# Kernel tuning notes

Hardware: AMD Instinct MI355X
Metric: run time of the kernel (lower is better)

## Reference

```python
import jax, jax.numpy as jnp
import numpy as np

B, T, D = 32, 200, 256
H, DH = 4, 32
INNER = H * DH  # 128
L, FF, NI = 8, 1024, 100000
NB = 64  # gap/recency buckets


def _ln(x, g, b, eps=1e-5):
    m = x.mean(-1, keepdims=True)
    v = jnp.mean((x - m) ** 2, -1, keepdims=True)
    return (x - m) / jnp.sqrt(v + eps) * g + b


def _gelu(x):
    return jax.nn.gelu(x, approximate=False)


def _dwconv_causal(x, w, b):
    # x: [B,T,C], w: [C,k] depthwise kernel, causal left-pad (k-1)
    k = w.shape[1]
    xp = jnp.pad(x, ((0, 0), (k - 1, 0), (0, 0))).transpose(0, 2, 1)  # [B,C,T+k-1]
    out = jax.lax.conv_general_dilated(
        xp, w[:, None, :], (1,), 'VALID',
        dimension_numbers=('NCH', 'OIH', 'NCH'), feature_group_count=w.shape[0])
    return out.transpose(0, 2, 1) + b


def _causal_linear_attention(q, k, v, m4):
    q = (jax.nn.elu(q) + 1.0) * m4
    k = (jax.nn.elu(k) + 1.0) * m4
    v = v * m4
    kv = jnp.einsum('bthd,bthe->bthde', k, v)          # [B,T,H,DH,DH]
    kv_prefix = jnp.cumsum(kv, axis=1)
    k_prefix = jnp.cumsum(k, axis=1)
    num = jnp.einsum('bthd,bthde->bthe', q, kv_prefix)
    den = jnp.sum(q * k_prefix, -1, keepdims=True)
    return num / (den + 1e-6) * m4


def _forward(item_emb, pos_emb, gap_emb, rec_emb, tf_w1, tf_b1, tf_w2, tf_b2,
             in_g, in_b, l_ln1g, l_ln1b, l_win, l_bin, l_wc, l_bc, l_tw, l_tb,
             l_pw, l_pb, l_wmix, l_bmix, l_ln2g, l_ln2b, l_wf1, l_bf1, l_wf2, l_bf2,
             fn_g, fn_b, pg_w, pg_b, uh_w1, uh_b1, uh_lng, uh_lnb, uh_w2, uh_b2,
             item_bias, ids, ts, lens):
    Bb, Tt = ids.shape
    pos = jnp.arange(Tt)
    mask = pos[None, :] >= (Tt - lens)[:, None]  # right-aligned valid mask [B,T]
    prev_ts = jnp.roll(ts, 1, axis=1)
    prev_mask = jnp.roll(mask, 1, axis=1).at[:, 0].set(False)
    zero = jnp.zeros_like(ts)
    gap_vals = jnp.where(mask & prev_mask, jnp.maximum(ts - prev_ts, 0), zero)
    latest = ts[:, -1:]
    rec_vals = jnp.where(mask, jnp.maximum(latest - ts, 0), zero)

    def buck(v, n):
        vf = jnp.maximum(v.astype(jnp.float32), 0.0)
        return jnp.clip(jnp.floor(jnp.log2(vf + 1.0)), 0, n - 1).astype(jnp.int32)

    gb = buck(gap_vals, NB)
    rb = buck(rec_vals, NB)
    rec_raw = jnp.maximum(latest - ts, 0).astype(jnp.float32)
    tf = jnp.stack([jnp.log1p(gb.astype(jnp.float32)), jnp.log1p(rec_raw)], -1)  # [B,T,2]
    dense_time = _gelu(tf @ tf_w1 + tf_b1) @ tf_w2 + tf_b2

    x = item_emb[ids] + pos_emb[None] + gap_emb[gb] + rec_emb[rb] + dense_time
    mf = mask[..., None].astype(x.dtype)
    m4 = mask[..., None, None].astype(x.dtype)
    x = _ln(x, in_g, in_b) * mf

    for i in range(L):
        res = x
        nrm = _ln(x, l_ln1g[i], l_ln1b[i])
        proj = nrm @ l_win[i] + l_bin[i]  # [B,T,D+3*INNER]
        gate = proj[..., :D]
        q = proj[..., D:D + INNER].reshape(Bb, Tt, H, DH)
        k = proj[..., D + INNER:D + 2 * INNER].reshape(Bb, Tt, H, DH)
        v = proj[..., D + 2 * INNER:].reshape(Bb, Tt, H, DH)
        content = _causal_linear_attention(q, k, v, m4).reshape(Bb, Tt, INNER) @ l_wc[i] + l_bc[i]
        temporal = _dwconv_causal(nrm, l_tw[i], l_tb[i])
        positional = _dwconv_causal(nrm, l_pw[i], l_pb[i])
        mixed = jnp.concatenate([content, temporal, positional], -1) @ l_wmix[i] + l_bmix[i]
        x = (res + jax.nn.sigmoid(gate) * mixed) * mf
        h = _ln(x, l_ln2g[i], l_ln2b[i])
        ffn = _gelu(h @ l_wf1[i] + l_bf1[i]) @ l_wf2[i] + l_bf2[i]
        x = (x + ffn) * mf

    x = _ln(x, fn_g, fn_b) * mf
    denom = jnp.maximum(lens, 1)[:, None].astype(x.dtype)
    mean_pooled = (x * mf).sum(1) / denom
    ps = (x @ pg_w + pg_b)[..., 0]
    ps = jnp.where(mask, ps, -1e9)
    pw = jax.nn.softmax(ps, axis=1)[..., None]
    attn_pooled = (pw * x).sum(1)
    last = x[:, -1, :]
    u = jnp.concatenate([last, mean_pooled, attn_pooled], -1)
    u = _gelu(u @ uh_w1 + uh_b1)
    u = _ln(u, uh_lng, uh_lnb)
    u = u @ uh_w2 + uh_b2
    u = u / jnp.maximum(jnp.linalg.norm(u, axis=-1, keepdims=True), 1e-12)
    ie = item_emb[1:]
    ie = ie / jnp.maximum(jnp.linalg.norm(ie, axis=-1, keepdims=True), 1e-12)
    return u @ ie.T + item_bias[1:]


def setup_inputs() -> dict:
    key = jax.random.key(0)
    it = iter(jax.random.split(key, 64))
    def nk():
        return next(it)
    def w(*s):
        return jax.random.normal(nk(), s, jnp.float32) * 0.02
    inp = dict(
        history_ids=jax.random.randint(nk(), (B, T), 0, NI),
        history_timestamps=jnp.sort(jax.random.randint(nk(), (B, T), 0, 1000000), axis=1),
        history_lengths=jax.random.randint(nk(), (B,), 1, T + 1),
        item_emb=w(NI + 1, D).at[0].set(0.0),
        pos_emb=w(T, D), gap_emb=w(NB, D), rec_emb=w(NB, D),
        tf_w1=w(2, D), tf_b1=jnp.zeros((D,)), tf_w2=w(D, D), tf_b2=jnp.zeros((D,)),
        in_g=jnp.ones((D,)), in_b=jnp.zeros((D,)),
        l_ln1g=jnp.ones((L, D)), l_ln1b=jnp.zeros((L, D)),
        l_win=w(L, D, D + 3 * INNER), l_bin=jnp.zeros((L, D + 3 * INNER)),
        l_wc=w(L, INNER, D), l_bc=jnp.zeros((L, D)),
        l_tw=w(L, D, 3), l_tb=jnp.zeros((L, D)),
        l_pw=w(L, D, 5), l_pb=jnp.zeros((L, D)),
        l_wmix=w(L, 3 * D, D), l_bmix=jnp.zeros((L, D)),
        l_ln2g=jnp.ones((L, D)), l_ln2b=jnp.zeros((L, D)),
        l_wf1=w(L, D, FF), l_bf1=jnp.zeros((L, FF)),
        l_wf2=w(L, FF, D), l_bf2=jnp.zeros((L, D)),
        fn_g=jnp.ones((D,)), fn_b=jnp.zeros((D,)),
        pg_w=w(D, 1), pg_b=jnp.zeros((1,)),
        uh_w1=w(3 * D, 1024), uh_b1=jnp.zeros((1024,)),
        uh_lng=jnp.ones((1024,)), uh_lnb=jnp.zeros((1024,)),
        uh_w2=w(1024, D), uh_b2=jnp.zeros((D,)),
        item_bias=jnp.zeros((NI + 1,)),
    )
    return inp


def reference(history_ids, history_timestamps, history_lengths, item_emb, pos_emb,
              gap_emb, rec_emb, tf_w1, tf_b1, tf_w2, tf_b2, in_g, in_b, l_ln1g,
              l_ln1b, l_win, l_bin, l_wc, l_bc, l_tw, l_tb, l_pw, l_pb, l_wmix,
              l_bmix, l_ln2g, l_ln2b, l_wf1, l_bf1, l_wf2, l_bf2, fn_g, fn_b,
              pg_w, pg_b, uh_w1, uh_b1, uh_lng, uh_lnb, uh_w2, uh_b2, item_bias):
    return _forward(item_emb, pos_emb, gap_emb, rec_emb, tf_w1, tf_b1, tf_w2, tf_b2,
                    in_g, in_b, l_ln1g, l_ln1b, l_win, l_bin, l_wc, l_bc, l_tw, l_tb,
                    l_pw, l_pb, l_wmix, l_bmix, l_ln2g, l_ln2b, l_wf1, l_bf1, l_wf2,
                    l_bf2, fn_g, fn_b, pg_w, pg_b, uh_w1, uh_b1, uh_lng, uh_lnb,
                    uh_w2, uh_b2, item_bias, history_ids, history_timestamps,
                    history_lengths)
```

## Files before the change

kernel.cpp:

```cpp
#include <hip/hip_runtime.h>
#include <math.h>

#define B_ 32
#define T_ 200
#define D_ 256
#define H_ 4
#define DH_ 32
#define INNER_ 128
#define L_ 8
#define FF_ 1024
#define NI_ 100000
#define NB_ 64
#define CH_ 25

typedef __attribute__((ext_vector_type(8))) short short8;
typedef __attribute__((ext_vector_type(8))) unsigned short ushort8;
typedef __attribute__((ext_vector_type(4))) unsigned short ushort4v;
typedef __attribute__((ext_vector_type(4))) float floatx4;

__device__ __forceinline__ float gelu_f(float x){
  return 0.5f*x*(1.0f+erff(x*0.70710678118654752f));
}
__device__ __forceinline__ float wsum(float v){
  #pragma unroll
  for (int o=32;o>0;o>>=1) v += __shfl_xor(v,o,64);
  return v;
}
__device__ __forceinline__ unsigned short f2bf(float x){
  unsigned int u = __float_as_uint(x);
  unsigned int r = (u + 0x7fffu + ((u>>16)&1u)) >> 16;
  return (unsigned short)r;
}
__device__ __forceinline__ float bf2f(unsigned short u){
  return __uint_as_float(((unsigned int)u)<<16);
}

__device__ __forceinline__ void cvt_tile(const float* __restrict__ src, unsigned short* __restrict__ dst,
                                         int K, int N, int tk, int tn, int tid, float (*s)[33])
{
  int tx = tid & 31, ty0 = tid >> 5;
  #pragma unroll
  for (int it=0; it<4; ++it){
    int ty = ty0 + it*8;
    s[ty][tx] = src[(size_t)(tk*32+ty)*N + tn*32+tx];
  }
  __syncthreads();
  #pragma unroll
  for (int it=0; it<4; ++it){
    int ty = ty0 + it*8;
    dst[(size_t)(tn*32+ty)*K + tk*32 + tx] = f2bf(s[tx][ty]);
  }
}

__global__ __launch_bounds__(256) void k_cvtAll(
  const float* __restrict__ win, const float* __restrict__ wmix,
  const float* __restrict__ wf1, const float* __restrict__ wf2,
  const float* __restrict__ tfw2, const float* __restrict__ uhw1, const float* __restrict__ uhw2,
  unsigned short* __restrict__ WtPerm, unsigned short* __restrict__ WtMixT,
  unsigned short* __restrict__ WtH,
  const float* __restrict__ bc, const float* __restrict__ bmix, float* __restrict__ bmixP)
{
  __shared__ float s[32][33];
  int b = blockIdx.x, tid = threadIdx.x;
  if (b < 6912){
    int l = b / 864, r = b % 864;
    if (r < 160)      cvt_tile(win + (size_t)l*163840, WtPerm + (size_t)l*688128,          256, 640,  r/20,      r%20,      tid, s);
    else if (r < 352){int t=r-160; cvt_tile(wmix + (size_t)l*196608, WtMixT + (size_t)l*196608, 768, 256, t/8, t%8, tid, s);}
    else if (r < 608){int t=r-352; cvt_tile(wf1 + (size_t)l*262144, WtPerm + (size_t)l*688128 + 163840, 256, 1024, t/32, t%32, tid, s);}
    else             {int t=r-608; cvt_tile(wf2 + (size_t)l*262144, WtPerm + (size_t)l*688128 + 425984, 1024, 256, t/8, t%8, tid, s);}
  } else if (b < 8000){
    int r = b - 6912;
    if (r < 64)       cvt_tile(tfw2, WtH,        256, 256,  r/8,  r%8,  tid, s);
    else if (r < 832){int t=r-64;  cvt_tile(uhw1, WtH+65536,  768, 1024, t/32, t%32, tid, s);}
    else             {int t=r-832; cvt_tile(uhw2, WtH+851968, 1024, 256, t/8,  t%8,  tid, s);}
  } else {
    int l = b - 8000; int n = tid;
    const float* w = wmix + (size_t)l*196608;
    const float* c = bc + l*256;
    float sum = bmix[l*256 + n];
    #pragma unroll 8
    for (int d=0; d<256; d++) sum += c[d]*w[(size_t)d*256 + n];
    bmixP[l*256+n] = sum;
  }
}

__global__ __launch_bounds__(256) void k_asm(
  const float* __restrict__ WcombF, const unsigned short* __restrict__ WtMixT,
  unsigned short* __restrict__ WtBig)
{
  int l = blockIdx.x >> 3, g = blockIdx.x & 7;
  int tid = threadIdx.x;
  int n = g*32 + (tid >> 3);
  int k0 = (tid & 7) * 80;
  const float* wc = WcombF + (size_t)l*32768;
  const unsigned short* wm = WtMixT + (size_t)l*196608 + (size_t)n*768;
  unsigned short* dst = WtBig + (size_t)l*163840 + (size_t)n*640;
  for (int kk=0; kk<80; kk++){
    int k = k0 + kk;
    dst[k] = (k < 128) ? f2bf(wc[(size_t)k*256 + n]) : wm[k+128];
  }
}

template<int TN>
__global__ __launch_bounds__(256) void k_gemm_bf(
    const float* __restrict__ A, const unsigned short* __restrict__ Wt,
    const float* __restrict__ bias, float* __restrict__ C,
    int M, int N, int K, int ldA, int ldW, int ldC, int mode,
    size_t sA, size_t sW, size_t sC, size_t sB)
{
  constexpr int NJ = TN/32;
  __shared__ unsigned short Als[128][40];
  __shared__ unsigned short Bls[TN][40];
  int z = blockIdx.z;
  A += (size_t)z*sA; Wt += (size_t)z*sW; C += (size_t)z*sC;
  const float* bz = bias ? bias + (size_t)z*sB : nullptr;
  int tid = threadIdx.x;
  int wave = tid >> 6, lane = tid & 63;
  int wm = (wave >> 1) * 64, wn = (wave & 1) * (TN/2);
  int frow = lane & 15, kg = lane >> 4;
  int bm = blockIdx.y * 128, bn = blockIdx.x * TN;
  int sm = tid >> 1, skh = (tid & 1) * 16;

  floatx4 acc[4][NJ];
  #pragma unroll
  for (int i=0;i<4;i++)
    #pragma unroll
    for (int j=0;j<NJ;j++) acc[i][j] = (floatx4){0.f,0.f,0.f,0.f};

  for (int k0=0; k0<K; k0+=32){
    {
      int gm = bm + sm;
      float f[16];
      if (gm < M){
        const float4* ap = (const float4*)(A + (size_t)gm*ldA + k0 + skh);
        #pragma unroll
        for (int c=0;c<4;c++){ float4 v = ap[c]; f[c*4]=v.x; f[c*4+1]=v.y; f[c*4+2]=v.z; f[c*4+3]=v.w; }
      } else {
        #pragma unroll
        for (int c=0;c<16;c++) f[c]=0.f;
      }
      ushort8 pa, pb;
      #pragma unroll
      for (int c=0;c<8;c++){ pa[c]=f2bf(f[c]); pb[c]=f2bf(f[8+c]); }
      *(ushort8*)&Als[sm][skh]   = pa;
      *(ushort8*)&Als[sm][skh+8] = pb;
    }
    #pragma unroll
    for (int u=0; u<TN/64; u++){
      int li = tid + u*256;
      int row = li >> 2, koff = (li & 3) * 8;
      int gn = bn + row;
      ushort8 wv;
      if (gn < N){
        wv = *(const ushort8*)&Wt[(size_t)gn*ldW + k0 + koff];
      } else {
        for (int c=0;c<8;c++) wv[c]=0;
      }
      *(ushort8*)&Bls[row][koff] = wv;
    }
    __syncthreads();
    short8 af[4], bf[NJ];
    #pragma unroll
    for (int i=0;i<4;i++) af[i] = *(const short8*)&Als[wm + 16*i + frow][kg*8];
    #pragma unroll
    for (int j=0;j<NJ;j++) bf[j] = *(const short8*)&Bls[wn + 16*j + frow][kg*8];
    #pragma unroll
    for (int i=0;i<4;i++)
      #pragma unroll
      for (int j=0;j<NJ;j++)
        acc[i][j] = __builtin_amdgcn_mfma_f32_16x16x32_bf16(af[i], bf[j], acc[i][j], 0, 0, 0);
    __syncthreads();
  }

  #pragma unroll
  for (int j=0;j<NJ;j++){
    int n = bn + wn + 16*j + frow;
    float bv = bz ? bz[n] : 0.f;
    #pragma unroll
    for (int i=0;i<4;i++){
      int m0 = bm + wm + 16*i + kg*4;
      #pragma unroll
      for (int r=0;r<4;r++){
        int m = m0 + r;
        if (m < M){
          float v = acc[i][j][r] + bv;
          if (mode == 1) v = gelu_f(v);
          float* cp = &C[(size_t)m*ldC + n];
          if (mode == 2) v += *cp;
          *cp = v;
        }
      }
    }
  }
}

template<int K, int NJ>
__global__ __launch_bounds__(256) void k_gemm16(
    const unsigned short* __restrict__ A, const unsigned short* __restrict__ Wt,
    const float* __restrict__ bias, void* __restrict__ Cv,
    int ldA, int ldW, int ldC, int mode)
{
  int tid = threadIdx.x;
  int wave = tid >> 6, lane = tid & 63;
  int frow = lane & 15, kg = lane >> 4;
  int bm = blockIdx.y * 32;
  int bn = blockIdx.x * (64*NJ) + wave * (16*NJ);

  const unsigned short* a0 = A + (size_t)(bm + frow)*ldA + kg*8;
  const unsigned short* a1 = a0 + (size_t)16*ldA;
  const unsigned short* b0 = Wt + (size_t)(bn + frow)*ldW + kg*8;

  floatx4 acc[2][NJ];
  #pragma unroll
  for (int i=0;i<2;i++)
    #pragma unroll
    for (int j=0;j<NJ;j++) acc[i][j] = (floatx4){0.f,0.f,0.f,0.f};

  #pragma unroll
  for (int k0=0; k0<K; k0+=32){
    short8 af0 = *(const short8*)(a0 + k0);
    short8 af1 = *(const short8*)(a1 + k0);
    #pragma unroll
    for (int j=0;j<NJ;j++){
      short8 bf = *(const short8*)(b0 + (size_t)j*16*ldW + k0);
      acc[0][j] = __builtin_amdgcn_mfma_f32_16x16x32_bf16(af0, bf, acc[0][j], 0, 0, 0);
      acc[1][j] = __builtin_amdgcn_mfma_f32_16x16x32_bf16(af1, bf, acc[1][j], 0, 0, 0);
    }
  }

  float* Cf = (float*)Cv;
  unsigned short* Ch = (unsigned short*)Cv;
  #pragma unroll
  for (int j=0;j<NJ;j++){
    int n = bn + 16*j + frow;
    float bv = bias[n];
    #pragma unroll
    for (int i=0;i<2;i++){
      int m0 = bm + 16*i + kg*4;
      #pragma unroll
      for (int r=0;r<4;r++){
        float v = acc[i][j][r] + bv;
        size_t off = (size_t)(m0+r)*ldC + n;
        if (mode == 1)      Cf[off] = gelu_f(v);
        else if (mode == 2) Cf[off] += v;
        else if (mode == 4) Ch[off] = f2bf(gelu_f(v));
        else                Cf[off] = v;
      }
    }
  }
}

__global__ __launch_bounds__(256) void k_proj(
  const unsigned short* __restrict__ A, const unsigned short* __restrict__ Wt,
  const float* __restrict__ bias, const int* __restrict__ lens,
  unsigned short* __restrict__ gateb, unsigned short* __restrict__ phiQ,
  unsigned short* __restrict__ phiK, unsigned short* __restrict__ vB,
  const float* __restrict__ tw, const float* __restrict__ tb,
  const float* __restrict__ pw, const float* __restrict__ pb,
  unsigned short* __restrict__ cat)
{
  int bid = blockIdx.x;
  int tid = threadIdx.x;
  if (bid < 400){
    int wave = tid >> 6, lane = tid & 63;
    int frow = lane & 15, kg = lane >> 4;
    int bx = bid & 1, by = bid >> 1;
    int bm = by * 32;
    int wn = bx*320 + wave*80;
    const unsigned short* a0 = A + (size_t)(bm + frow)*256 + kg*8;
    const unsigned short* a1 = a0 + (size_t)16*256;
    const unsigned short* b0 = Wt + (size_t)(wn + frow)*256 + kg*8;
    floatx4 acc[2][5];
    #pragma unroll
    for (int i=0;i<2;i++)
      #pragma unroll
      for (int j=0;j<5;j++) acc[i][j] = (floatx4){0.f,0.f,0.f,0.f};
    #pragma unroll
    for (int k0=0; k0<256; k0+=32){
      short8 af0 = *(const short8*)(a0 + k0);
      short8 af1 = *(const short8*)(a1 + k0);
      #pragma unroll
      for (int j=0;j<5;j++){
        short8 bf = *(const short8*)(b0 + (size_t)j*16*256 + k0);
        acc[0][j] = __builtin_amdgcn_mfma_f32_16x16x32_bf16(af0, bf, acc[0][j], 0, 0, 0);
        acc[1][j] = __builtin_amdgcn_mfma_f32_16x16x32_bf16(af1, bf, acc[1][j], 0, 0, 0);
      }
    }
    #pragma unroll
    for (int i=0;i<2;i++){
      #pragma unroll
      for (int r=0;r<4;r++){
        int row = bm + 16*i + kg*4 + r;
        int t = row % T_, b = row / T_;
        float m = (t >= T_ - lens[b]) ? 1.f : 0.f;
        #pragma unroll
        for (int j=0;j<5;j++){
          int n = wn + 16*j + frow;
          float v = acc[i][j][r] + bias[n];
          if (n < 256){
            gateb[(size_t)row*256 + n] = f2bf(v);
          } else if (n < 384){
            int bh = b*4 + ((n-256)>>5), dd = n & 31;
            phiQ[(size_t)bh*6400 + t*32 + dd] = f2bf((v > 0.f ? v + 1.f : __expf(v))*m);
          } else if (n < 512){
            int bh = b*4 + ((n-384)>>5), dd = n & 31;
            phiK[(size_t)bh*6400 + t*32 + dd] = f2bf((v > 0.f ? v + 1.f : __expf(v))*m);
          } else {
            int bh = b*4 + ((n-512)>>5), dd = n & 31;
            vB[(size_t)bh*6400 + t*32 + dd] = f2bf(v*m);
          }
        }
      }
    }
  } else {
    int bid2 = bid - 400;
    int d = tid;
    int bt0 = bid2*4;
    float xs8[8];
    #pragma unroll
    for (int w=0;w<8;w++){
      int wr = bt0 - 4 + w;
      xs8[w] = (wr >= 0) ? bf2f(A[(size_t)wr*256 + d]) : 0.f;
    }
    #pragma unroll
    for (int rr=0;rr<4;rr++){
      int bt = bt0 + rr, t = bt % T_;
      float ot = tb[d], op = pb[d];
      #pragma unroll
      for (int j=0;j<5;j++){
        int tt = t - 4 + j;
        float xv = (tt >= 0) ? xs8[rr+j] : 0.f;
        op += pw[d*5+j]*xv;
        if (j >= 2) ot += tw[d*3 + (j-2)]*xv;
      }
      cat[(size_t)bt*640 + 128 + d] = f2bf(ot);
      cat[(size_t)bt*640 + 384 + d] = f2bf(op);
    }
  }
}

template<int K, int MODE>
__global__ __launch_bounds__(256) void k_gemmln(
    const unsigned short* __restrict__ A, const unsigned short* __restrict__ Wt,
    const float* __restrict__ bias, float* __restrict__ xbuf,
    const unsigned short* __restrict__ gateb, const int* __restrict__ lens,
    const float* __restrict__ g, const float* __restrict__ bb,
    unsigned short* __restrict__ nrm, int maskLN)
{
  __shared__ float rs[16][4];
  __shared__ float rq[16][4];
  int tid = threadIdx.x;
  int wave = tid >> 6, lane = tid & 63;
  int frow = lane & 15, kg = lane >> 4;
  int bm = blockIdx.x * 16;
  int wn = wave * 64;

  const unsigned short* a0 = A + (size_t)(bm + frow)*K + kg*8;
  const unsigned short* b0 = Wt + (size_t)(wn + frow)*K + kg*8;

  floatx4 acc[4];
  #pragma unroll
  for (int j=0;j<4;j++) acc[j] = (floatx4){0.f,0.f,0.f,0.f};

  #pragma unroll
  for (int k0=0; k0<K; k0+=32){
    short8 af0 = *(const short8*)(a0 + k0);
    #pragma unroll
    for (int j=0;j<4;j++){
      short8 bf = *(const short8*)(b0 + (size_t)16*j*K + k0);
      acc[j] = __builtin_amdgcn_mfma_f32_16x16x32_bf16(af0, bf, acc[j], 0, 0, 0);
    }
  }

  float xn[4][4];
  float rowm[4];
  #pragma unroll
  for (int r=0;r<4;r++){
    int row = bm + kg*4 + r;
    int t = row % T_, b = row / T_;
    float m = (t >= T_ - lens[b]) ? 1.f : 0.f;
    rowm[r] = m;
    #pragma unroll
    for (int j=0;j<4;j++){
      int n = wn + 16*j + frow;
      float v = acc[j][r] + bias[n];
      float xv = xbuf[(size_t)row*256 + n];
      float xnv;
      if (MODE == 0){
        float gv = bf2f(gateb[(size_t)row*256 + n]);
        xnv = (xv + v/(1.f+__expf(-gv)))*m;
      } else {
        xnv = (xv + v)*m;
      }
      xn[j][r] = xnv;
      xbuf[(size_t)row*256 + n] = xnv;
    }
  }
  float mu[4];
  #pragma unroll
  for (int r=0;r<4;r++){
    float s = xn[0][r]+xn[1][r]+xn[2][r]+xn[3][r];
    s += __shfl_xor(s,1,64); s += __shfl_xor(s,2,64);
    s += __shfl_xor(s,4,64); s += __shfl_xor(s,8,64);
    if (frow == 0) rs[kg*4 + r][wave] = s;
  }
  __syncthreads();
  #pragma unroll
  for (int r=0;r<4;r++){
    int rl = kg*4 + r;
    mu[r] = (rs[rl][0]+rs[rl][1]+rs[rl][2]+rs[rl][3]) * (1.f/256.f);
  }
  float rstd[4];
  #pragma unroll
  for (int r=0;r<4;r++){
    float m0 = mu[r];
    float s = 0.f;
    #pragma unroll
    for (int j=0;j<4;j++){ float d = xn[j][r]-m0; s += d*d; }
    s += __shfl_xor(s,1,64); s += __shfl_xor(s,2,64);
    s += __shfl_xor(s,4,64); s += __shfl_xor(s,8,64);
    if (frow == 0) rq[kg*4 + r][wave] = s;
  }
  __syncthreads();
  #pragma unroll
  for (int r=0;r<4;r++){
    int rl = kg*4 + r;
    float q = rq[rl][0]+rq[rl][1]+rq[rl][2]+rq[rl][3];
    rstd[r] = rsqrtf(q*(1.f/256.f) + 1e-5f);
  }
  #pragma unroll
  for (int r=0;r<4;r++){
    int row = bm + kg*4 + r;
    float ml = maskLN ? rowm[r] : 1.f;
    #pragma unroll
    for (int j=0;j<4;j++){
      int n = wn + 16*j + frow;
      float h = (xn[j][r]-mu[r])*rstd[r]*g[n] + bb[n];
      nrm[(size_t)row*256 + n] = f2bf(h*ml);
    }
  }
}

__global__ __launch_bounds__(256) void k_embed(
  const int* __restrict__ ids, const int* __restrict__ ts, const int* __restrict__ lens,
  const float* __restrict__ item_emb, const float* __restrict__ pos_emb,
  const float* __restrict__ gap_emb, const float* __restrict__ rec_emb,
  const float* __restrict__ tf_w1, const float* __restrict__ tf_b1,
  float* __restrict__ xbuf, unsigned short* __restrict__ tfh)
{
  int bt = blockIdx.x;
  int b = bt / T_, t = bt % T_;
  int d = threadIdx.x;
  int len = lens[b];
  int tcur = ts[b*T_+t];
  int tlast = ts[b*T_+T_-1];
  bool mask  = t >= T_ - len;
  bool pmask = (t >= 1) && ((t-1) >= T_ - len);
  int gap = 0;
  if (mask && pmask){ int pv = ts[b*T_+t-1]; gap = max(tcur - pv, 0); }
  int rec = mask ? max(tlast - tcur, 0) : 0;
  int gb = min(max((int)floorf(log2f((float)gap + 1.0f)), 0), NB_-1);
  int rb = min(max((int)floorf(log2f((float)rec + 1.0f)), 0), NB_-1);
  float rec_raw = (float)max(tlast - tcur, 0);
  float tf0 = log1pf((float)gb);
  float tf1 = log1pf(rec_raw);
  float hid = gelu_f(tf0*tf_w1[d] + tf1*tf_w1[D_+d] + tf_b1[d]);
  tfh[(size_t)bt*D_ + d] = f2bf(hid);
  int id = ids[b*T_+t];
  xbuf[(size_t)bt*D_ + d] = item_emb[(size_t)id*D_ + d] + pos_emb[t*D_ + d]
                          + gap_emb[gb*D_ + d] + rec_emb[rb*D_ + d];
}

template<int NC>
__global__ __launch_bounds__(256) void k_ln(
  const float* __restrict__ in, void* __restrict__ out,
  const float* __restrict__ g, const float* __restrict__ bb,
  int rows, const int* __restrict__ lens, int applyMask, int outBf)
{
  int wid = threadIdx.x >> 6, lane = threadIdx.x & 63;
  int r = blockIdx.x*4 + wid;
  if (r >= rows) return;
  const int D = NC*256;
  const float4* rp = (const float4*)(in + (size_t)r*D);
  float4 v[NC];
  float s = 0.f;
  #pragma unroll
  for (int c=0;c<NC;c++){ v[c] = rp[c*64 + lane]; s += v[c].x+v[c].y+v[c].z+v[c].w; }
  s = wsum(s);
  float mean = s / (float)D;
  float q = 0.f;
  #pragma unroll
  for (int c=0;c<NC;c++){
    float a=v[c].x-mean, b2=v[c].y-mean, c2=v[c].z-mean, d2=v[c].w-mean;
    q += a*a + b2*b2 + c2*c2 + d2*d2;
  }
  q = wsum(q);
  float rstd = rsqrtf(q/(float)D + 1e-5f);
  float m = 1.f;
  if (applyMask){ int t = r % T_; int b = r / T_; m = (t >= T_ - lens[b]) ? 1.f : 0.f; }
  #pragma unroll
  for (int c=0;c<NC;c++){
    float4 gg  = ((const float4*)g )[c*64+lane];
    float4 bv  = ((const float4*)bb)[c*64+lane];
    float4 o;
    o.x = ((v[c].x-mean)*rstd*gg.x + bv.x)*m;
    o.y = ((v[c].y-mean)*rstd*gg.y + bv.y)*m;
    o.z = ((v[c].z-mean)*rstd*gg.z + bv.z)*m;
    o.w = ((v[c].w-mean)*rstd*gg.w + bv.w)*m;
    if (outBf){
      ushort4v ob; ob.x=f2bf(o.x); ob.y=f2bf(o.y); ob.z=f2bf(o.z); ob.w=f2bf(o.w);
      ((ushort4v*)((unsigned short*)out + (size_t)r*D))[c*64+lane] = ob;
    } else {
      ((float4*)((float*)out + (size_t)r*D))[c*64+lane] = o;
    }
  }
}

__global__ __launch_bounds__(256) void k_lnln(
  float* __restrict__ x, const int* __restrict__ lens,
  const float* __restrict__ g1, const float* __restrict__ b1,
  const float* __restrict__ g2, const float* __restrict__ b2,
  unsigned short* __restrict__ nrm)
{
  int wid = threadIdx.x >> 6, lane = threadIdx.x & 63;
  int r = blockIdx.x*4 + wid;
  int t = r % T_, b = r / T_;
  float m = (t >= T_ - lens[b]) ? 1.f : 0.f;
  float4 v = ((const float4*)(x + (size_t)r*256))[lane];
  float s = wsum(v.x+v.y+v.z+v.w);
  float mean = s/256.f;
  float a=v.x-mean, b2v=v.y-mean, c2=v.z-mean, d2=v.w-mean;
  float q = wsum(a*a+b2v*b2v+c2*c2+d2*d2);
  float rstd = rsqrtf(q/256.f + 1e-5f);
  float4 gg = ((const float4*)g1)[lane];
  float4 bv = ((const float4*)b1)[lane];
  float4 xn;
  xn.x = (a*rstd*gg.x + bv.x)*m;
  xn.y = (b2v*rstd*gg.y + bv.y)*m;
  xn.z = (c2*rstd*gg.z + bv.z)*m;
  xn.w = (d2*rstd*gg.w + bv.w)*m;
  ((float4*)(x + (size_t)r*256))[lane] = xn;
  float s2 = wsum(xn.x+xn.y+xn.z+xn.w);
  float mean2 = s2/256.f;
  float a2=xn.x-mean2, b22=xn.y-mean2, c22=xn.z-mean2, d22=xn.w-mean2;
  float q2 = wsum(a2*a2+b22*b22+c22*c22+d22*d22);
  float rstd2 = rsqrtf(q2/256.f + 1e-5f);
  float4 gg2 = ((const float4*)g2)[lane];
  float4 bv2 = ((const float4*)b2)[lane];
  ushort4v o;
  o.x = f2bf(a2*rstd2*gg2.x + bv2.x);
  o.y = f2bf(b22*rstd2*gg2.y + bv2.y);
  o.z = f2bf(c22*rstd2*gg2.z + bv2.z);
  o.w = f2bf(d22*rstd2*gg2.w + bv2.w);
  ((ushort4v*)(nrm + (size_t)r*256))[lane] = o;
}

__global__ __launch_bounds__(128) void k_attn_sums(
  const unsigned short* __restrict__ phiK, const unsigned short* __restrict__ vB,
  float* __restrict__ Ssum)
{
  int blk = blockIdx.x;
  int bh = blk >> 3, c = blk & 7;
  int tid = threadIdx.x; int e = tid & 31, q = tid >> 5;
  __shared__ float sk[CH_*32], sv[CH_*32];
  size_t base = (size_t)bh*6400 + (size_t)c*CH_*32;
  for (int idx = tid; idx < CH_*32; idx += 128){
    sk[idx] = bf2f(phiK[base + idx]);
    sv[idx] = bf2f(vB[base + idx]);
  }
  __syncthreads();
  float acc[8];
  #pragma unroll
  for (int j=0;j<8;j++) acc[j]=0.f;
  for (int tl=0; tl<CH_; tl++){
    const float4* k4 = (const float4*)(sk + tl*32 + q*8);
    float vf = sv[tl*32 + e];
    float4 ka = k4[0], kb = k4[1];
    acc[0]+=ka.x*vf; acc[1]+=ka.y*vf; acc[2]+=ka.z*vf; acc[3]+=ka.w*vf;
    acc[4]+=kb.x*vf; acc[5]+=kb.y*vf; acc[6]+=kb.z*vf; acc[7]+=kb.w*vf;
  }
  float* dst = Ssum + ((size_t)bh*8 + c)*1056;
  #pragma unroll
  for (int j=0;j<8;j++) dst[(q*8+j)*32 + e] = acc[j];
  if (q == 0){
    float s = 0.f;
    for (int tl=0; tl<CH_; tl++) s += sk[tl*32 + e];
    dst[1024 + e] = s;
  }
}

__global__ __launch_bounds__(256) void k_attn_out(
  const unsigned short* __restrict__ phiQ, const unsigned short* __restrict__ phiK,
  const unsigned short* __restrict__ vB, const int* __restrict__ lens,
  const float* __restrict__ Ssum, unsigned short* __restrict__ cat)
{
  int blk = blockIdx.x;
  int bh = blk >> 3, c = blk & 7;
  int b = bh >> 2, h = bh & 3;
  int tid = threadIdx.x; int e = tid & 31, qg = tid >> 5;
  int tstart = T_ - lens[b];
  __shared__ float sq[CH_*32], sk[CH_*32], sv[CH_*32];
  __shared__ float P[1056];
  __shared__ float A[CH_][CH_+1];
  __shared__ float sden[CH_];
  int t0 = c*CH_;
  const float* basep = Ssum + (size_t)bh*8*1056;
  for (int idx = tid; idx < 1056; idx += 256){
    float s = 0.f;
    for (int cp=0; cp<c; cp++) s += basep[(size_t)cp*1056 + idx];
    P[idx] = s;
  }
  size_t base = (size_t)bh*6400 + (size_t)c*CH_*32;
  for (int idx = tid; idx < CH_*32; idx += 256){
    sq[idx] = bf2f(phiQ[base + idx]);
    sk[idx] = bf2f(phiK[base + idx]);
    sv[idx] = bf2f(vB[base + idx]);
  }
  __syncthreads();
  for (int idx = tid; idx < CH_*CH_; idx += 256){
    int t = idx / CH_, tp = idx - t*CH_;
    float s = 0.f;
    if (tp <= t){
      const float4* q4 = (const float4*)(sq + t*32);
      const float4* k4 = (const float4*)(sk + tp*32);
      #pragma unroll
      for (int jj=0;jj<8;jj++){
        float4 qq = q4[jj], kk = k4[jj];
        s += qq.x*kk.x + qq.y*kk.y + qq.z*kk.z + qq.w*kk.w;
      }
    }
    A[t][tp] = s;
  }
  __syncthreads();
  if (tid < CH_){
    int t = tid;
    float s = 0.f;
    for (int tp=0; tp<=t; tp++) s += A[t][tp];
    const float* qf = sq + t*32;
    #pragma unroll
    for (int d=0; d<32; d++) s += qf[d]*P[1024+d];
    sden[t] = s;
  }
  __syncthreads();
  int tlo = (qg*CH_) >> 3, thi = ((qg+1)*CH_) >> 3;
  for (int t = tlo; t < thi; t++){
    float num = 0.f;
    for (int tp=0; tp<=t; tp++) num += A[t][tp]*sv[tp*32+e];
    const float* qf = sq + t*32;
    #pragma unroll
    for (int d=0; d<32; d++) num += qf[d]*P[d*32+e];
    int tg = t0 + t;
    float m = (tg >= tstart) ? 1.f : 0.f;
    cat[(size_t)(b*T_+tg)*640 + h*32 + e] = f2bf(num/(sden[t]+1e-6f)*m);
  }
}

__global__ __launch_bounds__(256) void k_pool(
  const unsigned short* __restrict__ x, const int* __restrict__ lens,
  const float* __restrict__ pg_w, const float* __restrict__ pg_b,
  float* __restrict__ u0)
{
  int b = blockIdx.x;
  int tid = threadIdx.x, wid = tid>>6, lane = tid&63;
  __shared__ float sps[T_];
  __shared__ float spw[T_];
  int len = lens[b]; int tstart = T_ - len;
  const float4* pw4 = (const float4*)pg_w;
  float4 wv = pw4[lane];
  for (int t = wid; t < T_; t += 4){
    ushort4v xv = ((const ushort4v*)(x + (size_t)(b*T_+t)*D_))[lane];
    float dot = bf2f(xv.x)*wv.x + bf2f(xv.y)*wv.y + bf2f(xv.z)*wv.z + bf2f(xv.w)*wv.w;
    dot = wsum(dot);
    if (lane==0) sps[t] = (t >= tstart) ? dot + pg_b[0] : -1e9f;
  }
  __syncthreads();
  float mx = -1e30f;
  for (int t=0;t<T_;t++) mx = fmaxf(mx, sps[t]);
  float sum = 0.f;
  for (int t=0;t<T_;t++) sum += __expf(sps[t]-mx);
  float inv = 1.f/sum;
  if (tid < T_) spw[tid] = __expf(sps[tid]-mx)*inv;
  __syncthreads();
  int d = tid;
  float macc=0.f, aacc=0.f;
  for (int t=0;t<T_;t++){
    float v = bf2f(x[(size_t)(b*T_+t)*D_ + d]);
    macc += v;
    aacc += spw[t]*v;
  }
  u0[b*768 + d]       = bf2f(x[(size_t)(b*T_+T_-1)*D_ + d]);
  u0[b*768 + 256 + d] = macc / (float)max(len,1);
  u0[b*768 + 512 + d] = aacc;
}

__global__ __launch_bounds__(64) void k_norm(float* __restrict__ u, unsigned short* __restrict__ ub)
{
  int b = blockIdx.x; int lane = threadIdx.x;
  float4* r = (float4*)(u + b*256);
  float4 v = r[lane];
  float ss = v.x*v.x + v.y*v.y + v.z*v.z + v.w*v.w;
  ss = wsum(ss);
  float sc = 1.f/fmaxf(sqrtf(ss), 1e-12f);
  v.x*=sc; v.y*=sc; v.z*=sc; v.w*=sc;
  r[lane]=v;
  ub[b*256 + lane*4 + 0] = f2bf(v.x);
  ub[b*256 + lane*4 + 1] = f2bf(v.y);
  ub[b*256 + lane*4 + 2] = f2bf(v.z);
  ub[b*256 + lane*4 + 3] = f2bf(v.w);
}

__global__ __launch_bounds__(256) void k_score2(
  const float* __restrict__ item_emb, const unsigned short* __restrict__ ub,
  const float* __restrict__ item_bias, float* __restrict__ out)
{
  int tid = threadIdx.x;
  int wave = tid >> 6, lane = tid & 63;
  int frow = lane & 15, kg = lane >> 4;
  int n0 = blockIdx.x * 128 + wave * 32;

  int g0 = n0 + frow, g1 = n0 + 16 + frow;
  bool ok0 = g0 < NI_, ok1 = g1 < NI_;
  const float* ip0 = item_emb + (size_t)(g0+1)*256 + kg*8;
  const float* ip1 = item_emb + (size_t)(g1+1)*256 + kg*8;
  const unsigned short* up0 = ub + frow*256 + kg*8;
  const unsigned short* up1 = up0 + 16*256;

  floatx4 acc[2][2];
  #pragma unroll
  for (int i=0;i<2;i++)
    #pragma unroll
    for (int j=0;j<2;j++) acc[i][j] = (floatx4){0.f,0.f,0.f,0.f};
  float ss0 = 0.f, ss1 = 0.f;

  #pragma unroll
  for (int k0=0; k0<256; k0+=32){
    float4 a0, a1, c0, c1;
    if (ok0){ a0 = *(const float4*)(ip0 + k0); a1 = *(const float4*)(ip0 + k0 + 4); }
    else    { a0 = (float4){0,0,0,0}; a1 = a0; }
    if (ok1){ c0 = *(const float4*)(ip1 + k0); c1 = *(const float4*)(ip1 + k0 + 4); }
    else    { c0 = (float4){0,0,0,0}; c1 = c0; }
    ss0 += a0.x*a0.x + a0.y*a0.y + a0.z*a0.z + a0.w*a0.w
         + a1.x*a1.x + a1.y*a1.y + a1.z*a1.z + a1.w*a1.w;
    ss1 += c0.x*c0.x + c0.y*c0.y + c0.z*c0.z + c0.w*c0.w
         + c1.x*c1.x + c1.y*c1.y + c1.z*c1.z + c1.w*c1.w;
    short8 af0, af1;
    af0[0]=(short)f2bf(a0.x); af0[1]=(short)f2bf(a0.y); af0[2]=(short)f2bf(a0.z); af0[3]=(short)f2bf(a0.w);
    af0[4]=(short)f2bf(a1.x); af0[5]=(short)f2bf(a1.y); af0[6]=(short)f2bf(a1.z); af0[7]=(short)f2bf(a1.w);
    af1[0]=(short)f2bf(c0.x); af1[1]=(short)f2bf(c0.y); af1[2]=(short)f2bf(c0.z); af1[3]=(short)f2bf(c0.w);
    af1[4]=(short)f2bf(c1.x); af1[5]=(short)f2bf(c1.y); af1[6]=(short)f2bf(c1.z); af1[7]=(short)f2bf(c1.w);
    short8 bf0 = *(const short8*)(up0 + k0);
    short8 bf1 = *(const short8*)(up1 + k0);
    acc[0][0] = __builtin_amdgcn_mfma_f32_16x16x32_bf16(af0, bf0, acc[0][0], 0, 0, 0);
    acc[0][1] = __builtin_amdgcn_mfma_f32_16x16x32_bf16(af0, bf1, acc[0][1], 0, 0, 0);
    acc[1][0] = __builtin_amdgcn_mfma_f32_16x16x32_bf16(af1, bf0, acc[1][0], 0, 0, 0);
    acc[1][1] = __builtin_amdgcn_mfma_f32_16x16x32_bf16(af1, bf1, acc[1][1], 0, 0, 0);
  }

  ss0 += __shfl_xor(ss0, 16, 64); ss0 += __shfl_xor(ss0, 32, 64);
  ss1 += __shfl_xor(ss1, 16, 64); ss1 += __shfl_xor(ss1, 32, 64);

  #pragma unroll
  for (int i=0;i<2;i++){
    int nb = n0 + 16*i + kg*4;
    if (nb >= NI_) continue;
    float ssr = i ? ss1 : ss0;
    float sc[4], bv[4];
    #pragma unroll
    for (int r=0;r<4;r++){
      float ssv = __shfl(ssr, kg*4 + r, 64);
      sc[r] = 1.f/fmaxf(sqrtf(ssv), 1e-12f);
      bv[r] = item_bias[nb + r + 1];
    }
    #pragma unroll
    for (int j=0;j<2;j++){
      int row = 16*j + frow;
      float4 o;
      o.x = acc[i][j][0]*sc[0] + bv[0];
      o.y = acc[i][j][1]*sc[1] + bv[1];
      o.z = acc[i][j][2]*sc[2] + bv[2];
      o.w = acc[i][j][3]*sc[3] + bv[3];
      *(float4*)&out[(size_t)row*NI_ + nb] = o;
    }
  }
}

extern "C" void kernel_launch(void* const* d_in, const int* in_sizes, int n_in,
                              void* d_out, int out_size, void* d_ws, size_t ws_size,
                              hipStream_t stream)
{
  const int* ids  = (const int*)d_in[0];
  const int* ts   = (const int*)d_in[1];
  const int* lens = (const int*)d_in[2];
  const float* item_emb = (const float*)d_in[3];
  const float* pos_emb  = (const float*)d_in[4];
  const float* gap_emb  = (const float*)d_in[5];
  const float* rec_emb  = (const float*)d_in[6];
  const float* tf_w1 = (const float*)d_in[7];
  const float* tf_b1 = (const float*)d_in[8];
  const float* tf_w2 = (const float*)d_in[9];
  const float* tf_b2 = (const float*)d_in[10];
  const float* in_g  = (const float*)d_in[11];
  const float* in_b  = (const float*)d_in[12];
  const float* l_ln1g = (const float*)d_in[13];
  const float* l_ln1b = (const float*)d_in[14];
  const float* l_win  = (const float*)d_in[15];
  const float* l_bin  = (const float*)d_in[16];
  const float* l_wc   = (const float*)d_in[17];
  const float* l_bc   = (const float*)d_in[18];
  const float* l_tw   = (const float*)d_in[19];
  const float* l_tb   = (const float*)d_in[20];
  const float* l_pw   = (const float*)d_in[21];
  const float* l_pb   = (const float*)d_in[22];
  const float* l_wmix = (const float*)d_in[23];
  const float* l_bmix = (const float*)d_in[24];
  const float* l_ln2g = (const float*)d_in[25];
  const float* l_ln2b = (const float*)d_in[26];
  const float* l_wf1  = (const float*)d_in[27];
  const float* l_bf1  = (const float*)d_in[28];
  const float* l_wf2  = (const float*)d_in[29];
  const float* l_bf2  = (const float*)d_in[30];
  const float* fn_g = (const float*)d_in[31];
  const float* fn_b = (const float*)d_in[32];
  const float* pg_w = (const float*)d_in[33];
  const float* pg_b = (const float*)d_in[34];
  const float* uh_w1 = (const float*)d_in[35];
  const float* uh_b1 = (const float*)d_in[36];
  const float* uh_lng = (const float*)d_in[37];
  const float* uh_lnb = (const float*)d_in[38];
  const float* uh_w2 = (const float*)d_in[39];
  const float* uh_b2 = (const float*)d_in[40];
  const float* item_bias = (const float*)d_in[41];
  float* out = (float*)d_out;

  const int MT = B_*T_;
  float* ws   = (float*)d_ws;
  float* xbuf = ws;
  float* tmp  = xbuf + (size_t)MT*D_;
  float* proj = tmp  + (size_t)MT*D_;
  float* cat  = proj + (size_t)MT*640;
  float* mid  = cat  + (size_t)MT*640;
  float* u0   = mid  + (size_t)MT*FF_;
  float* u1   = u0 + 32*768;
  float* u2   = u1 + 32*1024;
  float* WcombF = u2 + 32*256;
  float* bmixP  = WcombF + 262144;
  float* Ssum   = bmixP + 2048;
  unsigned short* WtPerm = (unsigned short*)(Ssum + 1081344);
  unsigned short* WtMixT = WtPerm + 5505024;
  unsigned short* WtBig  = WtMixT + 1572864;
  unsigned short* WtH    = WtBig  + 1310720;
  unsigned short* u2b    = WtH    + 1114112;

  unsigned short* tmpb = (unsigned short*)tmp;
  unsigned short* catb = (unsigned short*)cat;
  unsigned short* midb = (unsigned short*)(mid + (size_t)MT*D_);
  unsigned short* gateb = (unsigned short*)proj;
  unsigned short* phiQ  = gateb + 1638400;
  unsigned short* phiK  = phiQ + 819200;
  unsigned short* vBuf  = phiK + 819200;

  k_cvtAll<<<8008, 256, 0, stream>>>(l_win, l_wmix, l_wf1, l_wf2, tf_w2, uh_w1, uh_w2,
                                     WtPerm, WtMixT, WtH, l_bc, l_bmix, bmixP);
  k_gemm_bf<64><<<dim3(4,1,8), 256, 0, stream>>>(l_wc, WtMixT, nullptr, WcombF,
                                                 128, 256, 256, 256, 768, 256, 0,
                                                 (size_t)128*256, (size_t)196608, (size_t)32768, 0);
  k_asm<<<64, 256, 0, stream>>>(WcombF, WtMixT, WtBig);

  k_embed<<<MT, 256, 0, stream>>>(ids, ts, lens, item_emb, pos_emb, gap_emb, rec_emb,
                                  tf_w1, tf_b1, xbuf, tmpb);
  k_gemm16<256,2><<<dim3(2,200), 256, 0, stream>>>(tmpb, WtH, tf_b2, xbuf, 256, 256, 256, 2);
  k_lnln<<<MT/4, 256, 0, stream>>>(xbuf, lens, in_g, in_b, l_ln1g, l_ln1b, tmpb);

  for (int i=0;i<L_;i++){
    const unsigned short* WL = WtPerm + (size_t)i*688128;
    k_proj<<<2000, 256, 0, stream>>>(tmpb, WL, l_bin+i*640, lens,
                                     gateb, phiQ, phiK, vBuf,
                                     l_tw+i*768, l_tb+i*256, l_pw+i*1280, l_pb+i*256, catb);
    k_attn_sums<<<B_*H_*8, 128, 0, stream>>>(phiK, vBuf, Ssum);
    k_attn_out<<<B_*H_*8, 256, 0, stream>>>(phiQ, phiK, vBuf, lens, Ssum, catb);
    k_gemmln<640,0><<<400, 256, 0, stream>>>(catb, WtBig+(size_t)i*163840, bmixP+i*256,
                                             xbuf, gateb, lens,
                                             l_ln2g+i*256, l_ln2b+i*256, tmpb, 0);
    k_gemm16<256,4><<<dim3(4,200), 256, 0, stream>>>(tmpb, WL+163840, l_bf1+i*FF_, midb,
                                                     256, 256, FF_, 4);
    bool last = (i == L_-1);
    k_gemmln<1024,1><<<400, 256, 0, stream>>>(midb, WL+425984, l_bf2+i*256,
                                              xbuf, nullptr, lens,
                                              last ? fn_g : l_ln1g+(i+1)*256,
                                              last ? fn_b : l_ln1b+(i+1)*256,
                                              tmpb, last ? 1 : 0);
  }

  k_pool<<<B_, 256, 0, stream>>>(tmpb, lens, pg_w, pg_b, u0);
  k_gemm_bf<128><<<dim3(8,1), 256, 0, stream>>>(u0, WtH+65536, uh_b1, u1,
                                                32, 1024, 768, 768, 768, 1024, 1, 0,0,0,0);
  k_ln<4><<<8, 256, 0, stream>>>(u1, u1, uh_lng, uh_lnb, 32, lens, 0, 0);
  k_gemm_bf<64><<<dim3(4,1), 256, 0, stream>>>(u1, WtH+851968, uh_b2, u2,
                                               32, 256, 1024, 1024, 1024, 256, 0, 0,0,0,0);
  k_norm<<<B_, 64, 0, stream>>>(u2, u2b);

  k_score2<<<(NI_+127)/128, 256, 0, stream>>>(item_emb, u2b, item_bias, out);
}
```

Measured before the change: 1.687 ms.

## Fuse attention prefix-sum and output kernels; halve k_proj row tile

After: 1.735 ms. 1.03x slower.

```diff
diff --git a/kernel.cpp b/kernel.cpp
--- a/kernel.cpp
+++ b/kernel.cpp
@@ -261,59 +261,51 @@
 {
   int bid = blockIdx.x;
   int tid = threadIdx.x;
-  if (bid < 400){
+  if (bid < 800){
     int wave = tid >> 6, lane = tid & 63;
     int frow = lane & 15, kg = lane >> 4;
     int bx = bid & 1, by = bid >> 1;
-    int bm = by * 32;
+    int bm = by * 16;
     int wn = bx*320 + wave*80;
     const unsigned short* a0 = A + (size_t)(bm + frow)*256 + kg*8;
-    const unsigned short* a1 = a0 + (size_t)16*256;
     const unsigned short* b0 = Wt + (size_t)(wn + frow)*256 + kg*8;
-    floatx4 acc[2][5];
-    #pragma unroll
-    for (int i=0;i<2;i++)
-      #pragma unroll
-      for (int j=0;j<5;j++) acc[i][j] = (floatx4){0.f,0.f,0.f,0.f};
+    floatx4 acc[5];
+    #pragma unroll
+    for (int j=0;j<5;j++) acc[j] = (floatx4){0.f,0.f,0.f,0.f};
     #pragma unroll
     for (int k0=0; k0<256; k0+=32){
       short8 af0 = *(const short8*)(a0 + k0);
-      short8 af1 = *(const short8*)(a1 + k0);
       #pragma unroll
       for (int j=0;j<5;j++){
         short8 bf = *(const short8*)(b0 + (size_t)j*16*256 + k0);
-        acc[0][j] = __builtin_amdgcn_mfma_f32_16x16x32_bf16(af0, bf, acc[0][j], 0, 0, 0);
-        acc[1][j] = __builtin_amdgcn_mfma_f32_16x16x32_bf16(af1, bf, acc[1][j], 0, 0, 0);
+        acc[j] = __builtin_amdgcn_mfma_f32_16x16x32_bf16(af0, bf, acc[j], 0, 0, 0);
       }
     }
     #pragma unroll
-    for (int i=0;i<2;i++){
+    for (int r=0;r<4;r++){
+      int row = bm + kg*4 + r;
+      int t = row % T_, b = row / T_;
+      float m = (t >= T_ - lens[b]) ? 1.f : 0.f;
       #pragma unroll
-      for (int r=0;r<4;r++){
-        int row = bm + 16*i + kg*4 + r;
-        int t = row % T_, b = row / T_;
-        float m = (t >= T_ - lens[b]) ? 1.f : 0.f;
-        #pragma unroll
-        for (int j=0;j<5;j++){
-          int n = wn + 16*j + frow;
-          float v = acc[i][j][r] + bias[n];
-          if (n < 256){
-            gateb[(size_t)row*256 + n] = f2bf(v);
-          } else if (n < 384){
-            int bh = b*4 + ((n-256)>>5), dd = n & 31;
-            phiQ[(size_t)bh*6400 + t*32 + dd] = f2bf((v > 0.f ? v + 1.f : __expf(v))*m);
-          } else if (n < 512){
-            int bh = b*4 + ((n-384)>>5), dd = n & 31;
-            phiK[(size_t)bh*6400 + t*32 + dd] = f2bf((v > 0.f ? v + 1.f : __expf(v))*m);
-          } else {
-            int bh = b*4 + ((n-512)>>5), dd = n & 31;
-            vB[(size_t)bh*6400 + t*32 + dd] = f2bf(v*m);
-          }
+      for (int j=0;j<5;j++){
+        int n = wn + 16*j + frow;
+        float v = acc[j][r] + bias[n];
+        if (n < 256){
+          gateb[(size_t)row*256 + n] = f2bf(v);
+        } else if (n < 384){
+          int bh = b*4 + ((n-256)>>5), dd = n & 31;
+          phiQ[(size_t)bh*6400 + t*32 + dd] = f2bf((v > 0.f ? v + 1.f : __expf(v))*m);
+        } else if (n < 512){
+          int bh = b*4 + ((n-384)>>5), dd = n & 31;
+          phiK[(size_t)bh*6400 + t*32 + dd] = f2bf((v > 0.f ? v + 1.f : __expf(v))*m);
+        } else {
+          int bh = b*4 + ((n-512)>>5), dd = n & 31;
+          vB[(size_t)bh*6400 + t*32 + dd] = f2bf(v*m);
         }
       }
     }
   } else {
-    int bid2 = bid - 400;
+    int bid2 = bid - 800;
     int d = tid;
     int bt0 = bid2*4;
     float xs8[8];
@@ -336,6 +328,94 @@
       cat[(size_t)bt*640 + 128 + d] = f2bf(ot);
       cat[(size_t)bt*640 + 384 + d] = f2bf(op);
     }
+  }
+}
+
+__global__ __launch_bounds__(256) void k_attn_fused(
+  const unsigned short* __restrict__ phiQ, const unsigned short* __restrict__ phiK,
+  const unsigned short* __restrict__ vB, const int* __restrict__ lens,
+  unsigned short* __restrict__ cat)
+{
+  int blk = blockIdx.x;
+  int bh = blk >> 3, c = blk & 7;
+  int b = bh >> 2, h = bh & 3;
+  int tid = threadIdx.x; int e = tid & 31, qg = tid >> 5;
+  int tstart = T_ - lens[b];
+  __shared__ float sq[CH_*32], sk[CH_*32], sv[CH_*32];
+  __shared__ float P[1056];
+  __shared__ float A[CH_][CH_+1];
+  __shared__ float sden[CH_];
+  int t0 = c*CH_;
+  size_t bbase = (size_t)bh*6400;
+  float pkv0=0.f, pkv1=0.f, pkv2=0.f, pkv3=0.f, pks=0.f;
+  int dd = tid >> 3;
+  int e0 = (tid*4) & 31;
+  for (int cp=0; cp<c; cp++){
+    size_t pbase = bbase + (size_t)cp*800;
+    for (int idx=tid; idx<800; idx+=256){
+      sk[idx] = bf2f(phiK[pbase+idx]);
+      sv[idx] = bf2f(vB[pbase+idx]);
+    }
+    __syncthreads();
+    #pragma unroll 5
+    for (int tl=0; tl<CH_; tl++){
+      float kd = sk[tl*32+dd];
+      pkv0 += kd*sv[tl*32+e0];
+      pkv1 += kd*sv[tl*32+e0+1];
+      pkv2 += kd*sv[tl*32+e0+2];
+      pkv3 += kd*sv[tl*32+e0+3];
+    }
+    if (tid < 32){
+      float s = 0.f;
+      for (int tl=0; tl<CH_; tl++) s += sk[tl*32+tid];
+      pks += s;
+    }
+    __syncthreads();
+  }
+  P[tid*4+0]=pkv0; P[tid*4+1]=pkv1; P[tid*4+2]=pkv2; P[tid*4+3]=pkv3;
+  if (tid < 32) P[1024+tid] = pks;
+  size_t base = bbase + (size_t)c*800;
+  for (int idx=tid; idx<800; idx+=256){
+    sq[idx] = bf2f(phiQ[base+idx]);
+    sk[idx] = bf2f(phiK[base+idx]);
+    sv[idx] = bf2f(vB[base+idx]);
+  }
+  __syncthreads();
+  for (int idx = tid; idx < CH_*CH_; idx += 256){
+    int t = idx / CH_, tp = idx - t*CH_;
+    float s = 0.f;
+    if (tp <= t){
+      const float4* q4 = (const float4*)(sq + t*32);
+      const float4* k4 = (const float4*)(sk + tp*32);
+      #pragma unroll
+      for (int jj=0;jj<8;jj++){
+        float4 qq = q4[jj], kk = k4[jj];
+        s += qq.x*kk.x + qq.y*kk.y + qq.z*kk.z + qq.w*kk.w;
+      }
+    }
+    A[t][tp] = s;
+  }
+  __syncthreads();
+  if (tid < CH_){
+    int t = tid;
+    float s = 0.f;
+    for (int tp=0; tp<=t; tp++) s += A[t][tp];
+    const float* qf = sq + t*32;
+    #pragma unroll
+    for (int d=0; d<32; d++) s += qf[d]*P[1024+d];
+    sden[t] = s;
+  }
+  __syncthreads();
+  int tlo = (qg*CH_) >> 3, thi = ((qg+1)*CH_) >> 3;
+  for (int t = tlo; t < thi; t++){
+    float num = 0.f;
+    for (int tp=0; tp<=t; tp++) num += A[t][tp]*sv[tp*32+e];
+    const float* qf = sq + t*32;
+    #pragma unroll
+    for (int d=0; d<32; d++) num += qf[d]*P[d*32+e];
+    int tg = t0 + t;
+    float m = (tg >= tstart) ? 1.f : 0.f;
+    cat[(size_t)(b*T_+tg)*640 + h*32 + e] = f2bf(num/(sden[t]+1e-6f)*m);
   }
 }
 
@@ -553,106 +633,6 @@
   o.z = f2bf(c22*rstd2*gg2.z + bv2.z);
   o.w = f2bf(d22*rstd2*gg2.w + bv2.w);
   ((ushort4v*)(nrm + (size_t)r*256))[lane] = o;
-}
-
-__global__ __launch_bounds__(128) void k_attn_sums(
-  const unsigned short* __restrict__ phiK, const unsigned short* __restrict__ vB,
-  float* __restrict__ Ssum)
-{
-  int blk = blockIdx.x;
-  int bh = blk >> 3, c = blk & 7;
-  int tid = threadIdx.x; int e = tid & 31, q = tid >> 5;
-  __shared__ float sk[CH_*32], sv[CH_*32];
-  size_t base = (size_t)bh*6400 + (size_t)c*CH_*32;
-  for (int idx = tid; idx < CH_*32; idx += 128){
-    sk[idx] = bf2f(phiK[base + idx]);
-    sv[idx] = bf2f(vB[base + idx]);
-  }
-  __syncthreads();
-  float acc[8];
-  #pragma unroll
-  for (int j=0;j<8;j++) acc[j]=0.f;
-  for (int tl=0; tl<CH_; tl++){
-    const float4* k4 = (const float4*)(sk + tl*32 + q*8);
-    float vf = sv[tl*32 + e];
-    float4 ka = k4[0], kb = k4[1];
-    acc[0]+=ka.x*vf; acc[1]+=ka.y*vf; acc[2]+=ka.z*vf; acc[3]+=ka.w*vf;
-    acc[4]+=kb.x*vf; acc[5]+=kb.y*vf; acc[6]+=kb.z*vf; acc[7]+=kb.w*vf;
-  }
-  float* dst = Ssum + ((size_t)bh*8 + c)*1056;
-  #pragma unroll
-  for (int j=0;j<8;j++) dst[(q*8+j)*32 + e] = acc[j];
-  if (q == 0){
-    float s = 0.f;
-    for (int tl=0; tl<CH_; tl++) s += sk[tl*32 + e];
-    dst[1024 + e] = s;
-  }
-}
-
-__global__ __launch_bounds__(256) void k_attn_out(
-  const unsigned short* __restrict__ phiQ, const unsigned short* __restrict__ phiK,
-  const unsigned short* __restrict__ vB, const int* __restrict__ lens,
-  const float* __restrict__ Ssum, unsigned short* __restrict__ cat)
-{
-  int blk = blockIdx.x;
-  int bh = blk >> 3, c = blk & 7;
-  int b = bh >> 2, h = bh & 3;
-  int tid = threadIdx.x; int e = tid & 31, qg = tid >> 5;
-  int tstart = T_ - lens[b];
-  __shared__ float sq[CH_*32], sk[CH_*32], sv[CH_*32];
-  __shared__ float P[1056];
-  __shared__ float A[CH_][CH_+1];
-  __shared__ float sden[CH_];
-  int t0 = c*CH_;
-  const float* basep = Ssum + (size_t)bh*8*1056;
-  for (int idx = tid; idx < 1056; idx += 256){
-    float s = 0.f;
-    for (int cp=0; cp<c; cp++) s += basep[(size_t)cp*1056 + idx];
-    P[idx] = s;
-  }
-  size_t base = (size_t)bh*6400 + (size_t)c*CH_*32;
-  for (int idx = tid; idx < CH_*32; idx += 256){
-    sq[idx] = bf2f(phiQ[base + idx]);
-    sk[idx] = bf2f(phiK[base + idx]);
-    sv[idx] = bf2f(vB[base + idx]);
-  }
-  __syncthreads();
-  for (int idx = tid; idx < CH_*CH_; idx += 256){
-    int t = idx / CH_, tp = idx - t*CH_;
-    float s = 0.f;
-    if (tp <= t){
-      const float4* q4 = (const float4*)(sq + t*32);
-      const float4* k4 = (const float4*)(sk + tp*32);
-      #pragma unroll
-      for (int jj=0;jj<8;jj++){
-        float4 qq = q4[jj], kk = k4[jj];
-        s += qq.x*kk.x + qq.y*kk.y + qq.z*kk.z + qq.w*kk.w;
-      }
-    }
-    A[t][tp] = s;
-  }
-  __syncthreads();
-  if (tid < CH_){
-    int t = tid;
-    float s = 0.f;
-    for (int tp=0; tp<=t; tp++) s += A[t][tp];
-    const float* qf = sq + t*32;
-    #pragma unroll
-    for (int d=0; d<32; d++) s += qf[d]*P[1024+d];
-    sden[t] = s;
-  }
-  __syncthreads();
-  int tlo = (qg*CH_) >> 3, thi = ((qg+1)*CH_) >> 3;
-  for (int t = tlo; t < thi; t++){
-    float num = 0.f;
-    for (int tp=0; tp<=t; tp++) num += A[t][tp]*sv[tp*32+e];
-    const float* qf = sq + t*32;
-    #pragma unroll
-    for (int d=0; d<32; d++) num += qf[d]*P[d*32+e];
-    int tg = t0 + t;
-    float m = (tg >= tstart) ? 1.f : 0.f;
-    cat[(size_t)(b*T_+tg)*640 + h*32 + e] = f2bf(num/(sden[t]+1e-6f)*m);
-  }
 }
 
 __global__ __launch_bounds__(256) void k_pool(
@@ -873,17 +853,16 @@
 
   for (int i=0;i<L_;i++){
     const unsigned short* WL = WtPerm + (size_t)i*688128;
-    k_proj<<<2000, 256, 0, stream>>>(tmpb, WL, l_bin+i*640, lens,
+    bool last = (i == L_-1);
+    k_proj<<<2400, 256, 0, stream>>>(tmpb, WL, l_bin+i*640, lens,
                                      gateb, phiQ, phiK, vBuf,
                                      l_tw+i*768, l_tb+i*256, l_pw+i*1280, l_pb+i*256, catb);
-    k_attn_sums<<<B_*H_*8, 128, 0, stream>>>(phiK, vBuf, Ssum);
-    k_attn_out<<<B_*H_*8, 256, 0, stream>>>(phiQ, phiK, vBuf, lens, Ssum, catb);
+    k_attn_fused<<<B_*H_*8, 256, 0, stream>>>(phiQ, phiK, vBuf, lens, catb);
     k_gemmln<640,0><<<400, 256, 0, stream>>>(catb, WtBig+(size_t)i*163840, bmixP+i*256,
                                              xbuf, gateb, lens,
                                              l_ln2g+i*256, l_ln2b+i*256, tmpb, 0);
     k_gemm16<256,4><<<dim3(4,200), 256, 0, stream>>>(tmpb, WL+163840, l_bf1+i*FF_, midb,
                                                      256, 256, FF_, 4);
-    bool last = (i == L_-1);
     k_gemmln<1024,1><<<400, 256, 0, stream>>>(midb, WL+425984, l_bf2+i*256,
                                               xbuf, nullptr, lens,
                                               last ? fn_g : l_ln1g+(i+1)*256,
```
